# Kernel tuning notes

Measured on AMD Instinct MI355X. Metric: run time of the kernel, lower is better.

Reference implementation:

```python
import jax, jax.numpy as jnp
import numpy as np
import math

# Model dims
B, S, D, H = 2, 2048, 1024, 16
DH = D // H  # 64
TAU = 0.2
EPS = 1e-5

# Unit-scaling scale factors (constraint = gmean of fwd/bwd scales)
# Linear: gmean(fan_in**-0.5, fan_out**-0.5) = (fan_in*fan_out)**-0.25
# Matmul (m,k)@(k,n): gmean(k**-0.5, n**-0.5, m**-0.5) = (m*k*n)**(-1/6)
# Softmax over dim n: gmean(n/1.31, n/1.65) (empirical constants from unit_scaling)
# GELU: gmean(1/0.588, 1/0.675)
MM_SCALE = (S * S * DH) ** (-1.0 / 6.0)
SM_SCALE = S / math.sqrt(1.31 * 1.65)
GELU_SCALE = (0.588 * 0.675) ** -0.5
SQRT_TAU = math.sqrt(TAU)
SQRT_1MTAU = math.sqrt(1.0 - TAU)


def u_linear(x, w, b=None):
    fan_out, fan_in = w.shape
    scale = (fan_in * fan_out) ** -0.25
    y = x @ w.T
    if b is not None:
        y = y + b
    return y * scale


def layer_norm(x, w, b):
    m = jnp.mean(x, axis=-1, keepdims=True)
    v = jnp.mean(jnp.square(x - m), axis=-1, keepdims=True)
    return (x - m) * jax.lax.rsqrt(v + EPS) * w + b


def setup_inputs() -> dict:
    key = jax.random.key(0)
    ks = jax.random.split(key, 8)
    return {
        "x": jax.random.normal(ks[0], (B, S, D), jnp.float32),
        "w_qkv": jax.random.normal(ks[1], (3 * D, D), jnp.float32),
        "w_o": jax.random.normal(ks[2], (D, D), jnp.float32),
        "w1": jax.random.normal(ks[3], (4 * D, D), jnp.float32),
        "b1": jnp.zeros((4 * D,), jnp.float32),
        "w2": jax.random.normal(ks[4], (D, 4 * D), jnp.float32),
        "b2": jnp.zeros((D,), jnp.float32),
        "ln1_w": jnp.ones((D,), jnp.float32),
        "ln1_b": jnp.zeros((D,), jnp.float32),
        "ln2_w": jnp.ones((D,), jnp.float32),
        "ln2_b": jnp.zeros((D,), jnp.float32),
    }


def reference(x, w_qkv, w_o, w1, b1, w2, b2, ln1_w, ln1_b, ln2_w, ln2_b):
    # --- MHSA branch (residual_split forward is identity; tau enters at add) ---
    skip = x
    h = layer_norm(x, ln1_w, ln1_b)
    qkv = u_linear(h, w_qkv)  # [B,S,3D]
    # einops 'b s (d z h) -> z b h s d' with z=3, h=H
    qkv = qkv.reshape(B, S, DH, 3, H)
    q = jnp.transpose(qkv[:, :, :, 0, :], (0, 3, 1, 2))  # [B,H,S,DH]
    k = jnp.transpose(qkv[:, :, :, 1, :], (0, 3, 1, 2))
    v = jnp.transpose(qkv[:, :, :, 2, :], (0, 3, 1, 2))
    scores = jnp.einsum("bhsd,bhtd->bhst", q, k) * MM_SCALE
    attn = jax.nn.softmax(scores, axis=-1) * SM_SCALE
    # dropout: eval mode -> identity
    av = jnp.einsum("bhst,bhtd->bhsd", attn, v) * MM_SCALE
    av = jnp.transpose(av, (0, 2, 1, 3)).reshape(B, S, D)  # b h s d -> b s (h d)
    attn_out = u_linear(av, w_o)
    x = SQRT_TAU * attn_out + SQRT_1MTAU * skip  # residual_add

    # --- MLP branch ---
    skip = x
    h = layer_norm(x, ln2_w, ln2_b)
    h = u_linear(h, w1, b1)
    h = jax.nn.gelu(h, approximate=False) * GELU_SCALE
    h = u_linear(h, w2, b2)
    return SQRT_TAU * h + SQRT_1MTAU * skip
```

## Files before the change

### kernel.cpp

```cpp
#include <hip/hip_runtime.h>
#include <hip/hip_bf16.h>
#include <math.h>

typedef __hip_bfloat16 bf16;
typedef __attribute__((ext_vector_type(8))) short short8;
typedef __attribute__((ext_vector_type(4))) float floatx4;

#define B_   2
#define S_   2048
#define D_   1024
#define H_   16
#define DH_  64
#define BS_  4096
#define D3_  3072
#define DF_  4096

__device__ __forceinline__ float tof(float v) { return v; }
__device__ __forceinline__ float tof(bf16 v) { return __bfloat162float(v); }

__device__ __forceinline__ void gload_lds16(const bf16* g, bf16* l) {
  __builtin_amdgcn_global_load_lds(
      (const __attribute__((address_space(1))) unsigned int*)g,
      (__attribute__((address_space(3))) unsigned int*)l, 16, 0, 0);
}

#define VMCNT(n) asm volatile("s_waitcnt vmcnt(" #n ")" ::: "memory")

__global__ __launch_bounds__(256) void cvt_f32_bf16(
    const float* __restrict__ in, bf16* __restrict__ out, int n4) {
  int i = blockIdx.x * 256 + threadIdx.x;
  if (i >= n4) return;
  float4 v = ((const float4*)in)[i];
  bf16 o[4] = {__float2bfloat16(v.x), __float2bfloat16(v.y),
               __float2bfloat16(v.z), __float2bfloat16(v.w)};
  ((ulong1*)out)[i] = *(ulong1*)o;
}

__global__ __launch_bounds__(256) void cvt_qkv_o(
    const float* __restrict__ wqkv, const float* __restrict__ wo,
    bf16* __restrict__ wqb, bf16* __restrict__ wob) {
  const int g = blockIdx.x * 256 + threadIdx.x;
  if (g < 786432) {
    const int n2 = g >> 8;
    const int col = (g & 255) * 4;
    const int z = n2 >> 10, hh = (n2 >> 6) & 15, d = n2 & 63;
    const int n = d * 48 + z * 16 + hh;
    float4 v = *(const float4*)(wqkv + (size_t)n * 1024 + col);
    bf16 o[4] = {__float2bfloat16(v.x), __float2bfloat16(v.y),
                 __float2bfloat16(v.z), __float2bfloat16(v.w)};
    *(unsigned long long*)(wqb + (size_t)n2 * 1024 + col) =
        *(unsigned long long*)o;
  } else {
    const int g2 = g - 786432;
    float4 v = ((const float4*)wo)[g2];
    bf16 o[4] = {__float2bfloat16(v.x), __float2bfloat16(v.y),
                 __float2bfloat16(v.z), __float2bfloat16(v.w)};
    ((unsigned long long*)wob)[g2] = *(unsigned long long*)o;
  }
}

template <bool FUSE, bool INIT, typename TA, typename TS>
__global__ __launch_bounds__(256) void resid_ln_kernel(
    const TA* __restrict__ a, const TA* __restrict__ a2,
    const TS* __restrict__ skip,
    const float* __restrict__ w, const float* __restrict__ bias,
    bf16* __restrict__ hout, float st, float s1t,
    float* __restrict__ oinit, const float* __restrict__ b2,
    float cb, float cs) {
  const int row = blockIdx.x;
  const int tid = threadIdx.x;
  const int base = tid * 4;
  const size_t roff = (size_t)row * D_;

  float xv[4];
#pragma unroll
  for (int i = 0; i < 4; i++) {
    float v = tof(a[roff + base + i]);
    if (FUSE) v = st * (v + tof(a2[roff + base + i]))
                  + s1t * tof(skip[roff + base + i]);
    xv[i] = v;
  }
  if (INIT) {
#pragma unroll
    for (int i = 0; i < 4; i++)
      oinit[roff + base + i] = cs * xv[i] + cb * b2[base + i];
  }

  float ls = 0.f, lq = 0.f;
#pragma unroll
  for (int i = 0; i < 4; i++) { ls += xv[i]; lq += xv[i] * xv[i]; }

  __shared__ float ssum[256];
  __shared__ float ssq[256];
  ssum[tid] = ls; ssq[tid] = lq;
  __syncthreads();
  for (int off = 128; off > 0; off >>= 1) {
    if (tid < off) { ssum[tid] += ssum[tid + off]; ssq[tid] += ssq[tid + off]; }
    __syncthreads();
  }
  const float mean = ssum[0] * (1.0f / D_);
  const float var  = ssq[0] * (1.0f / D_) - mean * mean;
  const float rstd = rsqrtf(var + 1e-5f);

#pragma unroll
  for (int i = 0; i < 4; i++) {
    float v = (xv[i] - mean) * rstd * w[base + i] + bias[base + i];
    hout[roff + base + i] = __float2bfloat16(v);
  }
}

__global__ __launch_bounds__(256) void reduce_ffn2(
    const bf16* __restrict__ p0, const bf16* __restrict__ p1,
    float* __restrict__ out, float sc) {
  const size_t i = ((size_t)blockIdx.x * 256 + threadIdx.x) * 8;
  short8 a = *(const short8*)(p0 + i);
  short8 b = *(const short8*)(p1 + i);
  bf16 t0[8], t1[8];
  *(short8*)t0 = a; *(short8*)t1 = b;
  float4 o0 = *(float4*)(out + i);
  float4 o1 = *(float4*)(out + i + 4);
#pragma unroll
  for (int e = 0; e < 4; e++) {
    ((float*)&o0)[e] += sc * (__bfloat162float(t0[e]) + __bfloat162float(t1[e]));
    ((float*)&o1)[e] += sc * (__bfloat162float(t0[e + 4]) + __bfloat162float(t1[e + 4]));
  }
  *(float4*)(out + i) = o0;
  *(float4*)(out + i + 4) = o1;
}

template <int EPI, int NSPLIT, typename TC>
__global__ __launch_bounds__(512, 2) void gemm_mfma256(
    const bf16* __restrict__ A, const bf16* __restrict__ Bw,
    TC* __restrict__ C, int M, int N, int K, float scale,
    const float* __restrict__ bias, float st) {
  __shared__ __align__(16) bf16 As[2][2][128][64];
  __shared__ __align__(16) bf16 Bs[2][2][128][64];

  const int tid = threadIdx.x;
  const int lane = tid & 63;
  const int w = tid >> 6;
  const int wm = w >> 2;
  const int wn = w & 3;
  const int quad = lane >> 4;
  const int l16 = lane & 15;

  const int nbx = N >> 8;
  const int nwg = nbx * (M >> 8) * NSPLIT;
  int bid = blockIdx.x;
  bid = (bid & 7) * (nwg >> 3) + (bid >> 3);
  const int split = bid & (NSPLIT - 1);
  const int tile = bid / NSPLIT;
  const size_t bm = (size_t)(tile / nbx) * 256;
  const size_t bn = (size_t)(tile % nbx) * 256;
  const int lda = K * NSPLIT;
  const int koff = split * K;

  const bf16* gsrc[4][2];
  bf16* ldsp[4][2];
#pragma unroll
  for (int i = 0; i < 2; i++) {
    const int G = tid + i * 512;
    const int cr = G >> 3;
    const int gs8 = ((G & 7) ^ (cr & 7)) * 8;
    const int ra = ((cr >> 6) << 7) + (cr & 63);
    const int rb = ((cr >> 5) << 6) + (cr & 31);
    gsrc[0][i] = A  + (bm + ra) * (size_t)lda + koff + gs8;
    gsrc[2][i] = A  + (bm + ra + 64) * (size_t)lda + koff + gs8;
    gsrc[1][i] = Bw + (bn + rb) * (size_t)lda + koff + gs8;
    gsrc[3][i] = Bw + (bn + rb + 32) * (size_t)lda + koff + gs8;
    ldsp[0][i] = &As[0][0][0][0] + G * 8;
    ldsp[2][i] = &As[0][1][0][0] + G * 8;
    ldsp[1][i] = &Bs[0][0][0][0] + G * 8;
    ldsp[3][i] = &Bs[0][1][0][0] + G * 8;
  }

  auto STAGE = [&](int c, int tn) {
    const int boff = (tn & 1) * 16384;
    gload_lds16(gsrc[c][0] + (size_t)tn * 64, ldsp[c][0] + boff);
    gload_lds16(gsrc[c][1] + (size_t)tn * 64, ldsp[c][1] + boff);
  };

  const int ksw0 = (quad ^ (l16 & 7)) * 8;
  const int ksw1 = ((4 + quad) ^ (l16 & 7)) * 8;

  floatx4 acc[8][4];
#pragma unroll
  for (int i = 0; i < 8; i++)
#pragma unroll
    for (int j = 0; j < 4; j++) acc[i][j] = {0.f, 0.f, 0.f, 0.f};

  short8 af[4][2], bv[2][2];

  auto READ_A = [&](int b, int h) {
#pragma unroll
    for (int mf = 0; mf < 4; mf++) {
      const bf16* p = &As[b][h][wm * 64 + mf * 16 + l16][0];
      af[mf][0] = *(const short8*)(p + ksw0);
      af[mf][1] = *(const short8*)(p + ksw1);
    }
  };
  auto READ_B = [&](int b, int bh) {
#pragma unroll
    for (int nf = 0; nf < 2; nf++) {
      const bf16* p = &Bs[b][bh][wn * 32 + nf * 16 + l16][0];
      bv[nf][0] = *(const short8*)(p + ksw0);
      bv[nf][1] = *(const short8*)(p + ksw1);
    }
  };
  auto MFMA16 = [&](int mb, int nb) {
#pragma unroll
    for (int mf = 0; mf < 4; mf++)
#pragma unroll
      for (int nf = 0; nf < 2; nf++) {
        floatx4 c = acc[mb + mf][nb + nf];
        c = __builtin_amdgcn_mfma_f32_16x16x32_bf16(af[mf][0], bv[nf][0], c, 0, 0, 0);
        c = __builtin_amdgcn_mfma_f32_16x16x32_bf16(af[mf][1], bv[nf][1], c, 0, 0, 0);
        acc[mb + mf][nb + nf] = c;
      }
  };

  STAGE(0, 0); STAGE(1, 0); STAGE(2, 0); STAGE(3, 0);
  VMCNT(4);
  __builtin_amdgcn_s_barrier();
  __builtin_amdgcn_sched_barrier(0);

  const int NT = K >> 6;
#pragma unroll 1
  for (int t = 0; t < NT; t++) {
    const int b = t & 1;
    const bool nl = (t + 1 < NT);
    READ_A(b, 0);
    READ_B(b, 0);
    if (nl) STAGE(0, t + 1);
    __builtin_amdgcn_s_barrier();
    __builtin_amdgcn_sched_barrier(0);
    __builtin_amdgcn_s_setprio(1);
    MFMA16(0, 0);
    __builtin_amdgcn_s_setprio(0);
    if (nl) { VMCNT(2); } else { VMCNT(0); }
    __builtin_amdgcn_s_barrier();
    __builtin_amdgcn_sched_barrier(0);
    READ_B(b, 1);
    if (nl) STAGE(1, t + 1);
    __builtin_amdgcn_s_barrier();
    __builtin_amdgcn_sched_barrier(0);
    __builtin_amdgcn_s_setprio(1);
    MFMA16(0, 2);
    __builtin_amdgcn_s_setprio(0);
    __builtin_amdgcn_s_barrier();
    __builtin_amdgcn_sched_barrier(0);
    READ_A(b, 1);
    if (nl) STAGE(2, t + 1);
    __builtin_amdgcn_s_barrier();
    __builtin_amdgcn_sched_barrier(0);
    __builtin_amdgcn_s_setprio(1);
    MFMA16(4, 2);
    __builtin_amdgcn_s_setprio(0);
    __builtin_amdgcn_s_barrier();
    __builtin_amdgcn_sched_barrier(0);
    READ_B(b, 0);
    if (nl) STAGE(3, t + 1);
    __builtin_amdgcn_s_barrier();
    __builtin_amdgcn_sched_barrier(0);
    __builtin_amdgcn_s_setprio(1);
    MFMA16(4, 0);
    __builtin_amdgcn_s_setprio(0);
    if (nl) { VMCNT(4); } else { VMCNT(0); }
    __builtin_amdgcn_s_barrier();
    __builtin_amdgcn_sched_barrier(0);
  }

  float sc_eff = scale;
  if (EPI == 2) sc_eff = (bn < 1024) ? st : scale;
  float bias4[4];
  if (EPI == 1) {
#pragma unroll
    for (int j = 0; j < 4; j++) bias4[j] = bias[bn + wn * 64 + j * 16 + l16];
  }
#pragma unroll
  for (int mi = 0; mi < 8; mi++) {
    const size_t r0 = bm + wm * 128 + (mi >> 2) * 64 + (mi & 3) * 16 + quad * 4;
#pragma unroll
    for (int r = 0; r < 4; r++) {
      const size_t rowoff = (r0 + r) * (size_t)N + bn + wn * 64 + l16;
#pragma unroll
      for (int j = 0; j < 4; j++) {
        float v = acc[mi][j][r];
        if (EPI == 2 || EPI == 0) {
          ((bf16*)C)[rowoff + j * 16] = __float2bfloat16(v * sc_eff);
        } else {
          float u = (v + bias4[j]) * scale;
          float tt = u * (0.7978845608f + 0.0356774081f * u * u);
          float e = __builtin_amdgcn_exp2f(tt * 2.8853900818f);
          float th = 1.0f - 2.0f * __builtin_amdgcn_rcpf(e + 1.0f);
          ((bf16*)C)[rowoff + j * 16] =
              __float2bfloat16(0.5f * u * (1.0f + th) * st);
        }
      }
    }
  }
}

template <int EPI, typename TC>
__global__ __launch_bounds__(512, 2) void gemm_mfma128(
    const bf16* __restrict__ A, const bf16* __restrict__ Bw,
    TC* __restrict__ C, int M, int N, int K, float scale) {
  __shared__ __align__(16) bf16 As[2][2][128][64];
  __shared__ __align__(16) bf16 Bs[2][2][64][64];

  const int tid = threadIdx.x;
  const int lane = tid & 63;
  const int w = tid >> 6;
  const int wm = w >> 2;
  const int wn = w & 3;
  const int quad = lane >> 4;
  const int l16 = lane & 15;

  const int nbx = N >> 7;
  const int nwg = nbx * (M >> 8) * 2;
  int bid = blockIdx.x;
  bid = (bid & 7) * (nwg >> 3) + (bid >> 3);
  const int split = bid & 1;
  const int tile = bid >> 1;
  const size_t bm = (size_t)(tile / nbx) * 256;
  const size_t bn = (size_t)(tile % nbx) * 128;
  const int lda = K * 2;
  const int koff = split * K;

  const bf16* gA[2][2];
  bf16* lA[2][2];
#pragma unroll
  for (int i = 0; i < 2; i++) {
    const int G = tid + i * 512;
    const int cr = G >> 3;
    const int gs8 = ((G & 7) ^ (cr & 7)) * 8;
    const int ra = ((cr >> 6) << 7) + (cr & 63);
    gA[0][i] = A + (bm + ra) * (size_t)lda + koff + gs8;
    gA[1][i] = A + (bm + ra + 64) * (size_t)lda + koff + gs8;
    lA[0][i] = &As[0][0][0][0] + G * 8;
    lA[1][i] = &As[0][1][0][0] + G * 8;
  }
  const bf16* gB[2];
  bf16* lB[2];
  {
    const int cr = tid >> 3;
    const int gs8 = ((tid & 7) ^ (cr & 7)) * 8;
    gB[0] = Bw + (bn + cr) * (size_t)lda + koff + gs8;
    gB[1] = Bw + (bn + 64 + cr) * (size_t)lda + koff + gs8;
    lB[0] = &Bs[0][0][0][0] + tid * 8;
    lB[1] = &Bs[0][1][0][0] + tid * 8;
  }

  auto STAGE_A = [&](int h, int tn) {
    const int boff = (tn & 1) * 16384;
    gload_lds16(gA[h][0] + (size_t)tn * 64, lA[h][0] + boff);
    gload_lds16(gA[h][1] + (size_t)tn * 64, lA[h][1] + boff);
  };
  auto STAGE_B = [&](int bh, int tn) {
    const int boff = (tn & 1) * 8192;
    gload_lds16(gB[bh] + (size_t)tn * 64, lB[bh] + boff);
  };

  const int ksw0 = (quad ^ (l16 & 7)) * 8;
  const int ksw1 = ((4 + quad) ^ (l16 & 7)) * 8;

  floatx4 acc[8][2];
#pragma unroll
  for (int i = 0; i < 8; i++)
#pragma unroll
    for (int j = 0; j < 2; j++) acc[i][j] = {0.f, 0.f, 0.f, 0.f};

  short8 af[4][2], bv[2][2];

  auto READ_A = [&](int b, int h) {
#pragma unroll
    for (int mf = 0; mf < 4; mf++) {
      const bf16* p = &As[b][h][wm * 64 + mf * 16 + l16][0];
      af[mf][0] = *(const short8*)(p + ksw0);
      af[mf][1] = *(const short8*)(p + ksw1);
    }
  };
  auto READ_BNF = [&](int b, int nf) {
    const bf16* p = &Bs[b][wn >> 1][(wn & 1) * 32 + nf * 16 + l16][0];
    bv[nf][0] = *(const short8*)(p + ksw0);
    bv[nf][1] = *(const short8*)(p + ksw1);
  };
  auto MFMA8 = [&](int mb, int nf) {
#pragma unroll
    for (int mf = 0; mf < 4; mf++) {
      floatx4 c = acc[mb + mf][nf];
      c = __builtin_amdgcn_mfma_f32_16x16x32_bf16(af[mf][0], bv[nf][0], c, 0, 0, 0);
      c = __builtin_amdgcn_mfma_f32_16x16x32_bf16(af[mf][1], bv[nf][1], c, 0, 0, 0);
      acc[mb + mf][nf] = c;
    }
  };

  STAGE_A(0, 0); STAGE_B(0, 0); STAGE_B(1, 0); STAGE_A(1, 0);
  VMCNT(2);
  __builtin_amdgcn_s_barrier();
  __builtin_amdgcn_sched_barrier(0);

  const int NT = K >> 6;
#pragma unroll 1
  for (int t = 0; t < NT; t++) {
    const int b = t & 1;
    const bool nl = (t + 1 < NT);
    READ_A(b, 0);
    READ_BNF(b, 0);
    if (nl) STAGE_A(0, t + 1);
    __builtin_amdgcn_s_barrier();
    __builtin_amdgcn_sched_barrier(0);
    __builtin_amdgcn_s_setprio(1);
    MFMA8(0, 0);
    __builtin_amdgcn_s_setprio(0);
    __builtin_amdgcn_s_barrier();
    __builtin_amdgcn_sched_barrier(0);
    READ_BNF(b, 1);
    if (nl) STAGE_B(0, t + 1);
    __builtin_amdgcn_s_barrier();
    __builtin_amdgcn_sched_barrier(0);
    __builtin_amdgcn_s_setprio(1);
    MFMA8(0, 1);
    __builtin_amdgcn_s_setprio(0);
    if (nl) { VMCNT(3); } else { VMCNT(0); }
    __builtin_amdgcn_s_barrier();
    __builtin_amdgcn_sched_barrier(0);
    READ_A(b, 1);
    if (nl) STAGE_B(1, t + 1);
    __builtin_amdgcn_s_barrier();
    __builtin_amdgcn_sched_barrier(0);
    __builtin_amdgcn_s_setprio(1);
    MFMA8(4, 1);
    __builtin_amdgcn_s_setprio(0);
    __builtin_amdgcn_s_barrier();
    __builtin_amdgcn_sched_barrier(0);
    if (nl) STAGE_A(1, t + 1);
    __builtin_amdgcn_s_barrier();
    __builtin_amdgcn_sched_barrier(0);
    __builtin_amdgcn_s_setprio(1);
    MFMA8(4, 0);
    __builtin_amdgcn_s_setprio(0);
    if (nl) { VMCNT(2); } else { VMCNT(0); }
    __builtin_amdgcn_s_barrier();
    __builtin_amdgcn_sched_barrier(0);
  }

  const size_t poff = (size_t)split * M * N;
#pragma unroll
  for (int mi = 0; mi < 8; mi++) {
    const size_t r0 = bm + wm * 128 + (mi >> 2) * 64 + (mi & 3) * 16 + quad * 4;
#pragma unroll
    for (int r = 0; r < 4; r++) {
      const size_t rowoff = (r0 + r) * (size_t)N + bn + wn * 32 + l16;
#pragma unroll
      for (int j = 0; j < 2; j++) {
        float v = acc[mi][j][r];
        if (EPI == 3) {
          ((float*)C)[poff + rowoff + j * 16] = v * scale;
        } else {
          ((bf16*)C)[poff + rowoff + j * 16] = __float2bfloat16(v);
        }
      }
    }
  }
}

__global__ __launch_bounds__(512) void flash_attn_mfma(
    const bf16* __restrict__ qkv, bf16* __restrict__ att, float out_scale) {
  const int flat = (blockIdx.z * H_ + blockIdx.y) * (S_ / 128) + blockIdx.x;
  const int g8 = flat & 7, slot = flat >> 3;
  const int hf = g8 * 4 + (slot >> 4);
  const int qb = (slot & 15) * 128;
  const int h = hf & 15, b = hf >> 4;

  const int tid = threadIdx.x;
  const int lane = tid & 63;
  const int wv = tid >> 6;
  const int quad = lane >> 4;
  const int l16 = lane & 15;

  __shared__ __align__(16) bf16 Ks[2][64][64];
  __shared__ __align__(16) bf16 Vt[2][80][72];
  __shared__ __align__(16) bf16 Ps[128][64];

  const bf16* Qb_ = qkv + (size_t)b * S_ * D3_ + h * DH_;
  const bf16* Kb_ = Qb_ + 1024;
  const bf16* Vb_ = Qb_ + 2048;

  for (int i = tid; i < 2 * 16 * 72; i += 512) {
    const int bb = i / (16 * 72), rr = (i / 72) % 16, cc = i % 72;
    Vt[bb][64 + rr][cc] = __float2bfloat16(rr == 0 ? 1.f : 0.f);
  }

  short8 bq0, bq1;
  {
    const bf16* qrow = Qb_ + (size_t)(qb + wv * 16 + l16) * D3_ + quad * 8;
    bq0 = *(const short8*)(qrow);
    bq1 = *(const short8*)(qrow + 32);
  }

  floatx4 o[5];
#pragma unroll
  for (int fd = 0; fd < 5; fd++) o[fd] = {0.f, 0.f, 0.f, 0.f};

  const int prow = wv * 16 + l16;
  const int psw = (prow & 7) << 4;
  char* pbase = (char*)&Ps[0][0] + prow * 128;

  const bf16* ksrc =
      Kb_ + (size_t)(tid >> 3) * D3_ + (((tid & 7) ^ ((tid >> 3) & 7)) * 8);
  bf16* kdst = &Ks[0][0][0] + tid * 8;
  const int vj = tid & 63, vd = (tid >> 6) * 8;

  const int ksw0 = (quad ^ (l16 & 7)) * 8;
  const int ksw1 = ((4 + quad) ^ (l16 & 7)) * 8;

  gload_lds16(ksrc, kdst);
  uint4 vreg = *(const uint4*)(Vb_ + (size_t)vj * D3_ + vd);

  int cur = 0;
  for (int t = 0; t < S_ / 64; t++) {
    {
      bf16 tmp[8];
      *(uint4*)tmp = vreg;
#pragma unroll
      for (int e = 0; e < 8; e++) Vt[cur][vd + e][vj] = tmp[e];
    }
    __syncthreads();

    if (t + 1 < S_ / 64) {
      gload_lds16(ksrc + (size_t)(t + 1) * 64 * D3_, kdst + (cur ^ 1) * 4096);
      vreg = *(const uint4*)(Vb_ + (size_t)((t + 1) * 64 + vj) * D3_ + vd);
    }

    float st[4][4];
    __builtin_amdgcn_s_setprio(1);
#pragma unroll
    for (int fk = 0; fk < 4; fk++) {
      const bf16* kp = &Ks[cur][fk * 16 + l16][0];
      short8 ak0 = *(const short8*)(kp + ksw0);
      short8 ak1 = *(const short8*)(kp + ksw1);
      floatx4 acc = {0.f, 0.f, 0.f, 0.f};
      acc = __builtin_amdgcn_mfma_f32_16x16x32_bf16(ak0, bq0, acc, 0, 0, 0);
      acc = __builtin_amdgcn_mfma_f32_16x16x32_bf16(ak1, bq1, acc, 0, 0, 0);
#pragma unroll
      for (int r = 0; r < 4; r++) st[fk][r] = acc[r];
    }
    __builtin_amdgcn_s_setprio(0);

#pragma unroll
    for (int fk = 0; fk < 4; fk++) {
      bf16 pk[4];
#pragma unroll
      for (int r = 0; r < 4; r++)
        pk[r] = __float2bfloat16(__builtin_amdgcn_exp2f(st[fk][r]));
      *(uint2*)(pbase + ((fk * 32 + quad * 8) ^ psw)) = *(uint2*)pk;
    }

    short8 ap0 = *(const short8*)(pbase + ((quad * 16) ^ psw));
    short8 ap1 = *(const short8*)(pbase + ((64 + quad * 16) ^ psw));
    __builtin_amdgcn_s_setprio(1);
#pragma unroll
    for (int fd = 0; fd < 5; fd++) {
      short8 bv0 = *(const short8*)&Vt[cur][fd * 16 + l16][quad * 8];
      short8 bv1 = *(const short8*)&Vt[cur][fd * 16 + l16][32 + quad * 8];
      o[fd] = __builtin_amdgcn_mfma_f32_16x16x32_bf16(ap0, bv0, o[fd], 0, 0, 0);
      o[fd] = __builtin_amdgcn_mfma_f32_16x16x32_bf16(ap1, bv1, o[fd], 0, 0, 0);
    }
    __builtin_amdgcn_s_setprio(0);

    cur ^= 1;
  }

#pragma unroll
  for (int r = 0; r < 4; r++) {
    const float lq = __shfl(o[4][r], quad << 4, 64);
    const float sc = out_scale / lq;
    const size_t base =
        ((size_t)(b * S_ + qb + wv * 16 + quad * 4 + r)) * D_ + h * DH_;
#pragma unroll
    for (int fd = 0; fd < 4; fd++)
      att[base + fd * 16 + l16] = __float2bfloat16(o[fd][r] * sc);
  }
}

extern "C" void kernel_launch(void* const* d_in, const int* in_sizes, int n_in,
                              void* d_out, int out_size, void* d_ws, size_t ws_size,
                              hipStream_t stream) {
  const float* x     = (const float*)d_in[0];
  const float* w_qkv = (const float*)d_in[1];
  const float* w_o   = (const float*)d_in[2];
  const float* w1    = (const float*)d_in[3];
  const float* b1    = (const float*)d_in[4];
  const float* w2    = (const float*)d_in[5];
  const float* b2    = (const float*)d_in[6];
  const float* ln1w  = (const float*)d_in[7];
  const float* ln1b  = (const float*)d_in[8];
  const float* ln2w  = (const float*)d_in[9];
  const float* ln2b  = (const float*)d_in[10];
  float* out = (float*)d_out;
  bf16* ws  = (bf16*)d_ws;

  bf16* h1   = ws;
  bf16* wqb  = ws + 4194304;
  bf16* qkv  = ws + 8388608;
  bf16* att  = ws + 20971520;
  bf16* wob  = ws + 25165824;
  float* Po  = (float*)ws;
  bf16* w1b  = ws + 16777216;
  bf16* h2   = ws + 20971520;
  bf16* g    = ws;
  bf16* w2b  = ws + 16777216;
  bf16* Pf   = ws + 20971520;

  const float MM_SCALE   = (float)pow((double)S_ * S_ * DH_, -1.0 / 6.0);
  const float SM_SCALE   = (float)((double)S_ / sqrt(1.31 * 1.65));
  const float GELU_SCALE = (float)pow(0.588 * 0.675, -0.5);
  const float SQRT_TAU   = (float)sqrt(0.2);
  const float SQRT_1MT   = (float)sqrt(0.8);
  const float LOG2E      = 1.4426950408889634f;
  const float qkv_scale  = (float)pow((double)D_ * D3_, -0.25);
  const float o_scale    = (float)pow((double)D_ * D_, -0.25);
  const float w1_scale   = (float)pow((double)D_ * DF_, -0.25);
  const float w2_scale   = (float)pow((double)DF_ * D_, -0.25);

  cvt_qkv_o<<<4096, 256, 0, stream>>>(w_qkv, w_o, wqb, wob);
  resid_ln_kernel<false, false, float, float><<<BS_, 256, 0, stream>>>(
      x, nullptr, nullptr, ln1w, ln1b, h1, 0.f, 0.f, nullptr, nullptr, 0.f, 0.f);
  gemm_mfma256<2, 1, bf16><<<dim3(192), 512, 0, stream>>>(
      h1, wqb, qkv, BS_, D3_, D_, qkv_scale, nullptr,
      qkv_scale * MM_SCALE * LOG2E);
  flash_attn_mfma<<<dim3(S_ / 128, H_, B_), 512, 0, stream>>>(
      qkv, att, SM_SCALE * MM_SCALE);
  cvt_f32_bf16<<<(DF_ * D_ / 4 + 255) / 256, 256, 0, stream>>>(w1, w1b, DF_ * D_ / 4);
  gemm_mfma128<3, float><<<dim3(256), 512, 0, stream>>>(
      att, wob, Po, BS_, D_, D_ / 2, o_scale);
  resid_ln_kernel<true, true, float, float><<<BS_, 256, 0, stream>>>(
      Po, Po + (size_t)BS_ * D_, x, ln2w, ln2b, h2, SQRT_TAU, SQRT_1MT,
      out, b2, SQRT_TAU * w2_scale, SQRT_1MT);
  gemm_mfma256<1, 1, bf16><<<dim3(256), 512, 0, stream>>>(
      h2, w1b, g, BS_, DF_, D_, w1_scale, b1, GELU_SCALE);
  cvt_f32_bf16<<<(D_ * DF_ / 4 + 255) / 256, 256, 0, stream>>>(w2, w2b, D_ * DF_ / 4);
  gemm_mfma128<4, bf16><<<dim3(256), 512, 0, stream>>>(
      g, w2b, Pf, BS_, D_, DF_ / 2, 1.f);
  reduce_ffn2<<<2048, 256, 0, stream>>>(
      Pf, Pf + (size_t)BS_ * D_, out, SQRT_TAU * w2_scale);
}
```

Before: 348.4 us.

## Merge weight conversions, store out-proj partials in bf16, compute softmax denominator in registers

Folds the w1 conversion into the combined weight-cast kernel and moves the w2 cast earlier, reshuffling workspace buffers so they no longer conflict. The attention output-projection split-K partials are now stored as bf16 instead of fp32, which halves that intermediate traffic; the o_scale factor moves into the residual+LN kernel. Flash attention drops the extra ones-column MFMA used to accumulate the row sum and instead sums the probabilities in registers with shuffles. The exp stores are also interleaved with the first P fragment load. Storing partials in bf16 lowers precision.

New measurement: 338.7 us. 1.03x faster.

```diff
diff --git a/kernel.cpp b/kernel.cpp
--- a/kernel.cpp
+++ b/kernel.cpp
@@ -36,9 +36,10 @@
   ((ulong1*)out)[i] = *(ulong1*)o;
 }
 
-__global__ __launch_bounds__(256) void cvt_qkv_o(
+__global__ __launch_bounds__(256) void cvt_all(
     const float* __restrict__ wqkv, const float* __restrict__ wo,
-    bf16* __restrict__ wqb, bf16* __restrict__ wob) {
+    const float* __restrict__ w1, bf16* __restrict__ wqb,
+    bf16* __restrict__ wob, bf16* __restrict__ w1b) {
   const int g = blockIdx.x * 256 + threadIdx.x;
   if (g < 786432) {
     const int n2 = g >> 8;
@@ -50,12 +51,18 @@
                  __float2bfloat16(v.z), __float2bfloat16(v.w)};
     *(unsigned long long*)(wqb + (size_t)n2 * 1024 + col) =
         *(unsigned long long*)o;
-  } else {
+  } else if (g < 1048576) {
     const int g2 = g - 786432;
     float4 v = ((const float4*)wo)[g2];
     bf16 o[4] = {__float2bfloat16(v.x), __float2bfloat16(v.y),
                  __float2bfloat16(v.z), __float2bfloat16(v.w)};
     ((unsigned long long*)wob)[g2] = *(unsigned long long*)o;
+  } else {
+    const int g2 = g - 1048576;
+    float4 v = ((const float4*)w1)[g2];
+    bf16 o[4] = {__float2bfloat16(v.x), __float2bfloat16(v.y),
+                 __float2bfloat16(v.z), __float2bfloat16(v.w)};
+    ((unsigned long long*)w1b)[g2] = *(unsigned long long*)o;
   }
 }
 
@@ -128,7 +135,7 @@
   *(float4*)(out + i + 4) = o1;
 }
 
-template <int EPI, int NSPLIT, typename TC>
+template <int EPI, typename TC>
 __global__ __launch_bounds__(512, 2) void gemm_mfma256(
     const bf16* __restrict__ A, const bf16* __restrict__ Bw,
     TC* __restrict__ C, int M, int N, int K, float scale,
@@ -145,15 +152,11 @@
   const int l16 = lane & 15;
 
   const int nbx = N >> 8;
-  const int nwg = nbx * (M >> 8) * NSPLIT;
+  const int nwg = nbx * (M >> 8);
   int bid = blockIdx.x;
   bid = (bid & 7) * (nwg >> 3) + (bid >> 3);
-  const int split = bid & (NSPLIT - 1);
-  const int tile = bid / NSPLIT;
-  const size_t bm = (size_t)(tile / nbx) * 256;
-  const size_t bn = (size_t)(tile % nbx) * 256;
-  const int lda = K * NSPLIT;
-  const int koff = split * K;
+  const size_t bm = (size_t)(bid / nbx) * 256;
+  const size_t bn = (size_t)(bid % nbx) * 256;
 
   const bf16* gsrc[4][2];
   bf16* ldsp[4][2];
@@ -164,10 +167,10 @@
     const int gs8 = ((G & 7) ^ (cr & 7)) * 8;
     const int ra = ((cr >> 6) << 7) + (cr & 63);
     const int rb = ((cr >> 5) << 6) + (cr & 31);
-    gsrc[0][i] = A  + (bm + ra) * (size_t)lda + koff + gs8;
-    gsrc[2][i] = A  + (bm + ra + 64) * (size_t)lda + koff + gs8;
-    gsrc[1][i] = Bw + (bn + rb) * (size_t)lda + koff + gs8;
-    gsrc[3][i] = Bw + (bn + rb + 32) * (size_t)lda + koff + gs8;
+    gsrc[0][i] = A  + (bm + ra) * (size_t)K + gs8;
+    gsrc[2][i] = A  + (bm + ra + 64) * (size_t)K + gs8;
+    gsrc[1][i] = Bw + (bn + rb) * (size_t)K + gs8;
+    gsrc[3][i] = Bw + (bn + rb + 32) * (size_t)K + gs8;
     ldsp[0][i] = &As[0][0][0][0] + G * 8;
     ldsp[2][i] = &As[0][1][0][0] + G * 8;
     ldsp[1][i] = &Bs[0][0][0][0] + G * 8;
@@ -286,7 +289,7 @@
 #pragma unroll
       for (int j = 0; j < 4; j++) {
         float v = acc[mi][j][r];
-        if (EPI == 2 || EPI == 0) {
+        if (EPI == 2) {
           ((bf16*)C)[rowoff + j * 16] = __float2bfloat16(v * sc_eff);
         } else {
           float u = (v + bias4[j]) * scale;
@@ -301,10 +304,9 @@
   }
 }
 
-template <int EPI, typename TC>
 __global__ __launch_bounds__(512, 2) void gemm_mfma128(
     const bf16* __restrict__ A, const bf16* __restrict__ Bw,
-    TC* __restrict__ C, int M, int N, int K, float scale) {
+    bf16* __restrict__ C, bf16* __restrict__ C2, int M, int N, int K) {
   __shared__ __align__(16) bf16 As[2][2][128][64];
   __shared__ __align__(16) bf16 Bs[2][2][64][64];
 
@@ -445,7 +447,7 @@
     __builtin_amdgcn_sched_barrier(0);
   }
 
-  const size_t poff = (size_t)split * M * N;
+  bf16* dst = split ? C2 : C;
 #pragma unroll
   for (int mi = 0; mi < 8; mi++) {
     const size_t r0 = bm + wm * 128 + (mi >> 2) * 64 + (mi & 3) * 16 + quad * 4;
@@ -453,14 +455,8 @@
     for (int r = 0; r < 4; r++) {
       const size_t rowoff = (r0 + r) * (size_t)N + bn + wn * 32 + l16;
 #pragma unroll
-      for (int j = 0; j < 2; j++) {
-        float v = acc[mi][j][r];
-        if (EPI == 3) {
-          ((float*)C)[poff + rowoff + j * 16] = v * scale;
-        } else {
-          ((bf16*)C)[poff + rowoff + j * 16] = __float2bfloat16(v);
-        }
-      }
+      for (int j = 0; j < 2; j++)
+        dst[rowoff + j * 16] = __float2bfloat16(acc[mi][j][r]);
     }
   }
 }
@@ -480,17 +476,12 @@
   const int l16 = lane & 15;
 
   __shared__ __align__(16) bf16 Ks[2][64][64];
-  __shared__ __align__(16) bf16 Vt[2][80][72];
+  __shared__ __align__(16) bf16 Vt[2][64][72];
   __shared__ __align__(16) bf16 Ps[128][64];
 
   const bf16* Qb_ = qkv + (size_t)b * S_ * D3_ + h * DH_;
   const bf16* Kb_ = Qb_ + 1024;
   const bf16* Vb_ = Qb_ + 2048;
-
-  for (int i = tid; i < 2 * 16 * 72; i += 512) {
-    const int bb = i / (16 * 72), rr = (i / 72) % 16, cc = i % 72;
-    Vt[bb][64 + rr][cc] = __float2bfloat16(rr == 0 ? 1.f : 0.f);
-  }
 
   short8 bq0, bq1;
   {
@@ -499,9 +490,10 @@
     bq1 = *(const short8*)(qrow + 32);
   }
 
-  floatx4 o[5];
-#pragma unroll
-  for (int fd = 0; fd < 5; fd++) o[fd] = {0.f, 0.f, 0.f, 0.f};
+  float l_part = 0.f;
+  floatx4 o[4];
+#pragma unroll
+  for (int fd = 0; fd < 4; fd++) o[fd] = {0.f, 0.f, 0.f, 0.f};
 
   const int prow = wv * 16 + l16;
   const int psw = (prow & 7) << 4;
@@ -549,19 +541,33 @@
     __builtin_amdgcn_s_setprio(0);
 
 #pragma unroll
-    for (int fk = 0; fk < 4; fk++) {
+    for (int fk = 0; fk < 2; fk++) {
       bf16 pk[4];
 #pragma unroll
-      for (int r = 0; r < 4; r++)
-        pk[r] = __float2bfloat16(__builtin_amdgcn_exp2f(st[fk][r]));
+      for (int r = 0; r < 4; r++) {
+        const float p = __builtin_amdgcn_exp2f(st[fk][r]);
+        l_part += p;
+        pk[r] = __float2bfloat16(p);
+      }
       *(uint2*)(pbase + ((fk * 32 + quad * 8) ^ psw)) = *(uint2*)pk;
     }
-
     short8 ap0 = *(const short8*)(pbase + ((quad * 16) ^ psw));
+#pragma unroll
+    for (int fk = 2; fk < 4; fk++) {
+      bf16 pk[4];
+#pragma unroll
+      for (int r = 0; r < 4; r++) {
+        const float p = __builtin_amdgcn_exp2f(st[fk][r]);
+        l_part += p;
+        pk[r] = __float2bfloat16(p);
+      }
+      *(uint2*)(pbase + ((fk * 32 + quad * 8) ^ psw)) = *(uint2*)pk;
+    }
     short8 ap1 = *(const short8*)(pbase + ((64 + quad * 16) ^ psw));
-    __builtin_amdgcn_s_setprio(1);
-#pragma unroll
-    for (int fd = 0; fd < 5; fd++) {
+
+    __builtin_amdgcn_s_setprio(1);
+#pragma unroll
+    for (int fd = 0; fd < 4; fd++) {
       short8 bv0 = *(const short8*)&Vt[cur][fd * 16 + l16][quad * 8];
       short8 bv1 = *(const short8*)&Vt[cur][fd * 16 + l16][32 + quad * 8];
       o[fd] = __builtin_amdgcn_mfma_f32_16x16x32_bf16(ap0, bv0, o[fd], 0, 0, 0);
@@ -572,9 +578,11 @@
     cur ^= 1;
   }
 
+  l_part += __shfl_xor(l_part, 16);
+  l_part += __shfl_xor(l_part, 32);
 #pragma unroll
   for (int r = 0; r < 4; r++) {
-    const float lq = __shfl(o[4][r], quad << 4, 64);
+    const float lq = __shfl(l_part, quad * 4 + r, 64);
     const float sc = out_scale / lq;
     const size_t base =
         ((size_t)(b * S_ + qb + wv * 16 + quad * 4 + r)) * D_ + h * DH_;
@@ -603,15 +611,16 @@
 
   bf16* h1   = ws;
   bf16* wqb  = ws + 4194304;
+  bf16* wob  = ws + 7340032;
   bf16* qkv  = ws + 8388608;
   bf16* att  = ws + 20971520;
-  bf16* wob  = ws + 25165824;
-  float* Po  = (float*)ws;
-  bf16* w1b  = ws + 16777216;
-  bf16* h2   = ws + 20971520;
-  bf16* g    = ws;
-  bf16* w2b  = ws + 16777216;
-  bf16* Pf   = ws + 20971520;
+  bf16* w1b  = ws + 25165824;
+  bf16* w2b  = ws;
+  bf16* Po   = ws + 8388608;
+  bf16* h2   = ws + 4194304;
+  bf16* g    = ws + 8388608;
+  bf16* Pf0  = ws + 4194304;
+  bf16* Pf1  = ws + 25165824;
 
   const float MM_SCALE   = (float)pow((double)S_ * S_ * DH_, -1.0 / 6.0);
   const float SM_SCALE   = (float)((double)S_ / sqrt(1.31 * 1.65));
@@ -624,25 +633,23 @@
   const float w1_scale   = (float)pow((double)D_ * DF_, -0.25);
   const float w2_scale   = (float)pow((double)DF_ * D_, -0.25);
 
-  cvt_qkv_o<<<4096, 256, 0, stream>>>(w_qkv, w_o, wqb, wob);
+  cvt_all<<<8192, 256, 0, stream>>>(w_qkv, w_o, w1, wqb, wob, w1b);
   resid_ln_kernel<false, false, float, float><<<BS_, 256, 0, stream>>>(
       x, nullptr, nullptr, ln1w, ln1b, h1, 0.f, 0.f, nullptr, nullptr, 0.f, 0.f);
-  gemm_mfma256<2, 1, bf16><<<dim3(192), 512, 0, stream>>>(
+  gemm_mfma256<2, bf16><<<dim3(192), 512, 0, stream>>>(
       h1, wqb, qkv, BS_, D3_, D_, qkv_scale, nullptr,
       qkv_scale * MM_SCALE * LOG2E);
+  cvt_f32_bf16<<<4096, 256, 0, stream>>>(w2, w2b, D_ * DF_ / 4);
   flash_attn_mfma<<<dim3(S_ / 128, H_, B_), 512, 0, stream>>>(
       qkv, att, SM_SCALE * MM_SCALE);
-  cvt_f32_bf16<<<(DF_ * D_ / 4 + 255) / 256, 256, 0, stream>>>(w1, w1b, DF_ * D_ / 4);
-  gemm_mfma128<3, float><<<dim3(256), 512, 0, stream>>>(
-      att, wob, Po, BS_, D_, D_ / 2, o_scale);
-  resid_ln_kernel<true, true, float, float><<<BS_, 256, 0, stream>>>(
-      Po, Po + (size_t)BS_ * D_, x, ln2w, ln2b, h2, SQRT_TAU, SQRT_1MT,
-      out, b2, SQRT_TAU * w2_scale, SQRT_1MT);
-  gemm_mfma256<1, 1, bf16><<<dim3(256), 512, 0, stream>>>(
+  gemm_mfma128<<<dim3(256), 512, 0, stream>>>(
+      att, wob, Po, Po + (size_t)BS_ * D_, BS_, D_, D_ / 2);
+  resid_ln_kernel<true, true, bf16, float><<<BS_, 256, 0, stream>>>(
+      Po, Po + (size_t)BS_ * D_, x, ln2w, ln2b, h2,
+      SQRT_TAU * o_scale, SQRT_1MT, out, b2, SQRT_TAU * w2_scale, SQRT_1MT);
+  gemm_mfma256<1, bf16><<<dim3(256), 512, 0, stream>>>(
       h2, w1b, g, BS_, DF_, D_, w1_scale, b1, GELU_SCALE);
-  cvt_f32_bf16<<<(D_ * DF_ / 4 + 255) / 256, 256, 0, stream>>>(w2, w2b, D_ * DF_ / 4);
-  gemm_mfma128<4, bf16><<<dim3(256), 512, 0, stream>>>(
-      g, w2b, Pf, BS_, D_, DF_ / 2, 1.f);
-  reduce_ffn2<<<2048, 256, 0, stream>>>(
-      Pf, Pf + (size_t)BS_ * D_, out, SQRT_TAU * w2_scale);
-}
+  gemm_mfma128<<<dim3(256), 512, 0, stream>>>(
+      g, w2b, Pf0, Pf1, BS_, D_, DF_ / 2);
+  reduce_ffn2<<<2048, 256, 0, stream>>>(Pf0, Pf1, out, SQRT_TAU * w2_scale);
+}
```
